# Kernel tuning notes

Measured on AMD Instinct MI355X. Metric: run time of the kernel, lower is better.

The kernel has to match this reference:

```python
import jax, jax.numpy as jnp
import numpy as np

EPS = 1e-8  # torch F.cosine_similarity eps


def _gather(features, idx):
    # batched_index_select_tensor: per-batch gather along seq dim
    return jnp.take_along_axis(features, idx[:, :, None], axis=1)


def setup_inputs() -> dict:
    key = jax.random.key(0)
    ks = jax.random.split(key, 7)
    B, S, H, Q, D, C = 8, 512, 768, 64, 256, 2
    return {
        "features": jax.random.normal(ks[0], (B, S, H), dtype=jnp.float32),
        "text_a_indices": jax.random.randint(ks[1], (B, Q), 0, S),
        "text_b_indices": jax.random.randint(ks[2], (B, D), 0, S),
        "W1": jax.random.normal(ks[3], (2 * H, H), dtype=jnp.float32) * 0.02,
        "b1": jax.random.normal(ks[4], (H,), dtype=jnp.float32) * 0.02,
        "W2": jax.random.normal(ks[5], (H, C), dtype=jnp.float32) * 0.02,
        "b2": jax.random.normal(ks[6], (C,), dtype=jnp.float32) * 0.02,
    }


def reference(features, text_a_indices, text_b_indices, W1, b1, W2, b2):
    dt = features.dtype
    a_mask = (text_a_indices > 0).astype(dt)          # [B,Q]
    b_mask = (text_b_indices > 0).astype(dt)          # [B,D]
    a_len = jnp.sum(a_mask, axis=-1)                  # [B]
    b_len = jnp.sum(b_mask, axis=-1)                  # [B]

    q_vec = _gather(features, text_a_indices)         # [B,Q,H]
    d_vec = _gather(features, text_b_indices)         # [B,D,H]

    # cosine similarity with torch eps semantics: x.y / (max(|x|,eps)*max(|y|,eps))
    qn = q_vec / jnp.maximum(jnp.linalg.norm(q_vec, axis=-1, keepdims=True), EPS)
    dn = d_vec / jnp.maximum(jnp.linalg.norm(d_vec, axis=-1, keepdims=True), EPS)
    sim = jnp.einsum("bqh,bdh->bqd", qn, dn)          # [B,Q,D]

    # masked weighted average over doc tokens, per query token (fused; no 4D repeat)
    sim_m = sim * b_mask[:, None, :]
    per_q_doc = jnp.einsum("bqd,bdh->bqh", sim_m, d_vec) / b_len[:, None, None]

    # masked average over query tokens
    am = a_mask[:, :, None]
    query_based_doc = jnp.sum(per_q_doc * am, axis=1) / a_len[:, None]   # [B,H]
    query_avg = jnp.sum(q_vec * am, axis=1) / a_len[:, None]             # [B,H]

    feat = jnp.concatenate([query_avg, query_based_doc], axis=-1)        # [B,2H]
    hidden = jax.nn.relu(feat @ W1 + b1)
    logits = hidden @ W2 + b2
    return logits
```

## Files before the change

### kernel.cpp

```cpp
#include <hip/hip_runtime.h>
#include <hip/hip_bf16.h>

#define B_ 8
#define S_ 512
#define H_ 768
#define Q_ 64
#define D_ 256

#define WS_QBAR   0
#define WS_QA     (B_ * H_)
#define WS_W      (2 * B_ * H_)
#define WS_HIDDEN (2 * B_ * H_ + B_ * D_)
#define WS_CNT    (WS_HIDDEN + B_ * H_)
#define ZERO_N    (B_ * H_ + 256)

__global__ __launch_bounds__(256) void k_qbar(
        const float* __restrict__ feats,
        const int* __restrict__ aidx,
        float* __restrict__ ws) {
    float* qbar = ws + WS_QBAR;
    float* qa   = ws + WS_QA;
    int b = blockIdx.x / 12, hc = blockIdx.x % 12;
    int t = threadIdx.x, wv = t >> 6, lane = t & 63;
    __shared__ float s_alen;
    __shared__ float red0[4][64], red1[4][64];
    if (wv == 0) {
        unsigned long long ma = __ballot(aidx[b * Q_ + lane] > 0);
        if (lane == 0) s_alen = (float)__popcll(ma);
    }
    int hh = hc * 64 + lane;
    float pb = 0.f, pa = 0.f;
#pragma unroll 2
    for (int q = wv * 16; q < wv * 16 + 16; ++q) {
        int idx = aidx[b * Q_ + q];
        const float* row = feats + ((size_t)b * S_ + idx) * H_;
        const float4* row4 = (const float4*)row;
        float ss = 0.f;
#pragma unroll
        for (int k = 0; k < 3; ++k) {
            float4 v = row4[lane + k * 64];
            ss += v.x * v.x + v.y * v.y + v.z * v.z + v.w * v.w;
        }
        for (int off = 32; off; off >>= 1) ss += __shfl_xor(ss, off, 64);
        float inv = 1.f / fmaxf(sqrtf(ss), 1e-8f);
        float f = row[hh];
        if (idx > 0) { pb += f * inv; pa += f; }
    }
    red0[wv][lane] = pb;
    red1[wv][lane] = pa;
    __syncthreads();
    if (t < 64) {
        int h2 = hc * 64 + t;
        float qb = red0[0][t] + red0[1][t] + red0[2][t] + red0[3][t];
        float qv = red1[0][t] + red1[1][t] + red1[2][t] + red1[3][t];
        qbar[b * H_ + h2] = qb;
        qa[b * H_ + h2] = qv / s_alen;
    }
}

__global__ __launch_bounds__(256) void k_docw(
        const float* __restrict__ feats,
        const int* __restrict__ aidx,
        const int* __restrict__ bidx,
        float* __restrict__ ws) {
    const float* qbar = ws + WS_QBAR;
    float* w = ws + WS_W;
    float* zero_region = ws + WS_HIDDEN;
    int t = threadIdx.x, wv = t >> 6, lane = t & 63;
    if (blockIdx.x < 25) {
        zero_region[blockIdx.x * 256 + t] = 0.f;
    }
    int gw = blockIdx.x * 4 + wv;
    int b = gw >> 8, d = gw & 255;
    __shared__ int cnt[4];
    __shared__ float s_alen;
    unsigned long long mb = __ballot(bidx[b * D_ + wv * 64 + lane] > 0);
    if (lane == 0) cnt[wv] = __popcll(mb);
    if (wv == 0) {
        unsigned long long ma = __ballot(aidx[b * Q_ + lane] > 0);
        if (lane == 0) s_alen = (float)__popcll(ma);
    }
    __syncthreads();
    float blen = (float)(cnt[0] + cnt[1] + cnt[2] + cnt[3]);
    int idx = bidx[b * D_ + d];
    const float4* row4 = (const float4*)(feats + ((size_t)b * S_ + idx) * H_);
    const float4* q4 = (const float4*)(qbar + b * H_);
    float dqf = 0.f, dff = 0.f;
#pragma unroll
    for (int k = 0; k < 3; ++k) {
        float4 v = row4[lane + k * 64];
        float4 qv = q4[lane + k * 64];
        dqf += v.x * qv.x + v.y * qv.y + v.z * qv.z + v.w * qv.w;
        dff += v.x * v.x + v.y * v.y + v.z * v.z + v.w * v.w;
    }
    for (int off = 32; off; off >>= 1) {
        dqf += __shfl_xor(dqf, off, 64);
        dff += __shfl_xor(dff, off, 64);
    }
    if (lane == 0) {
        float inv = 1.f / fmaxf(sqrtf(dff), 1e-8f);
        float scale = 1.f / (s_alen * blen);
        w[b * D_ + d] = (idx > 0) ? dqf * inv * scale : 0.f;
    }
}

__global__ __launch_bounds__(256) void k_docsum_mlp(
        const float* __restrict__ feats,
        const int* __restrict__ bidx,
        const float* __restrict__ W1,
        const float* __restrict__ b1,
        const float* __restrict__ W2,
        const float* __restrict__ b2,
        float* __restrict__ ws,
        float* __restrict__ out) {
    const float* qa = ws + WS_QA;
    const float* w  = ws + WS_W;
    float* hidden   = ws + WS_HIDDEN;
    int* counter    = (int*)(ws + WS_CNT);
    int b = blockIdx.x / 12, hc = blockIdx.x % 12;
    int t = threadIdx.x, wv = t >> 6, lane = t & 63;
    __shared__ float s_w[D_];
    __shared__ int   s_i[D_];
    __shared__ float s_k[128];
    __shared__ float red[4][64];
    __shared__ int   s_flag;
    s_w[t] = w[b * D_ + t];
    s_i[t] = bidx[b * D_ + t];
    if (t < 64) s_k[t] = qa[b * H_ + hc * 64 + t];
    __syncthreads();
    int hh = hc * 64 + lane;
    float acc = 0.f;
#pragma unroll 8
    for (int d = wv * 64; d < wv * 64 + 64; ++d)
        acc += s_w[d] * feats[((size_t)b * S_ + s_i[d]) * H_ + hh];
    red[wv][lane] = acc;
    __syncthreads();
    if (t < 64) s_k[64 + t] = red[0][t] + red[1][t] + red[2][t] + red[3][t];
    __syncthreads();
    const float* Wtop = W1 + (size_t)(hc * 64) * H_;
    const float* Wbot = W1 + (size_t)(H_ + hc * 64) * H_;
    float h0 = 0.f, h1 = 0.f, h2 = 0.f;
#pragma unroll 4
    for (int i = 0; i < 64; ++i) {
        float ka = s_k[i], kb = s_k[64 + i];
        const float* r1 = Wtop + (size_t)i * H_;
        const float* r2 = Wbot + (size_t)i * H_;
        h0 += ka * r1[t]       + kb * r2[t];
        h1 += ka * r1[t + 256] + kb * r2[t + 256];
        h2 += ka * r1[t + 512] + kb * r2[t + 512];
    }
    atomicAdd(&hidden[b * H_ + t],       h0);
    atomicAdd(&hidden[b * H_ + t + 256], h1);
    atomicAdd(&hidden[b * H_ + t + 512], h2);
    __threadfence();
    __syncthreads();
    if (t == 0) {
        int old = atomicAdd(counter, 1);
        s_flag = (old == 95);
    }
    __syncthreads();
    if (s_flag) {
        __threadfence();
        for (int bb = wv * 2; bb < wv * 2 + 2; ++bb) {
            float a0 = 0.f, a1 = 0.f;
#pragma unroll
            for (int k = 0; k < 12; ++k) {
                int h = lane + k * 64;
                float hv = __hip_atomic_load(&hidden[bb * H_ + h],
                                             __ATOMIC_RELAXED,
                                             __HIP_MEMORY_SCOPE_AGENT);
                float v = fmaxf(hv + b1[h], 0.f);
                a0 += v * W2[h * 2 + 0];
                a1 += v * W2[h * 2 + 1];
            }
            for (int off = 32; off; off >>= 1) {
                a0 += __shfl_xor(a0, off, 64);
                a1 += __shfl_xor(a1, off, 64);
            }
            if (lane == 0) {
                out[bb * 2 + 0] = a0 + b2[0];
                out[bb * 2 + 1] = a1 + b2[1];
            }
        }
    }
}

extern "C" void kernel_launch(void* const* d_in, const int* in_sizes, int n_in,
                              void* d_out, int out_size, void* d_ws, size_t ws_size,
                              hipStream_t stream) {
    const float* feats = (const float*)d_in[0];
    const int*   aidx  = (const int*)d_in[1];
    const int*   bidx  = (const int*)d_in[2];
    const float* W1    = (const float*)d_in[3];
    const float* b1    = (const float*)d_in[4];
    const float* W2    = (const float*)d_in[5];
    const float* b2    = (const float*)d_in[6];
    float* out = (float*)d_out;
    float* ws = (float*)d_ws;

    k_qbar<<<96, 256, 0, stream>>>(feats, aidx, ws);
    k_docw<<<512, 256, 0, stream>>>(feats, aidx, bidx, ws);
    k_docsum_mlp<<<96, 256, 0, stream>>>(feats, bidx, W1, b1, W2, b2, ws, out);
}
```

Measured before the change: 113.3 us.

## Fuse query, doc-weight and MLP stages into one kernel with redundant per-block work

Merges the three kernels into a single 512-thread kernel per (batch, hidden-chunk) block. Each block recomputes the full query-norm sum and all 256 doc weights itself rather than reading them from workspace written by earlier launches. The atomic hidden accumulation and last-block counter are replaced by per-chunk partial sums that a small tail kernel reduces. This removes launch overhead, the atomics and the workspace zeroing, at the cost of each batch's gathers being repeated 12 times across blocks.

```diff
diff --git a/kernel.cpp b/kernel.cpp
--- a/kernel.cpp
+++ b/kernel.cpp
@@ -6,182 +6,172 @@
 #define H_ 768
 #define Q_ 64
 #define D_ 256
+#define EPSF 1e-8f
 
-#define WS_QBAR   0
-#define WS_QA     (B_ * H_)
-#define WS_W      (2 * B_ * H_)
-#define WS_HIDDEN (2 * B_ * H_ + B_ * D_)
-#define WS_CNT    (WS_HIDDEN + B_ * H_)
-#define ZERO_N    (B_ * H_ + 256)
-
-__global__ __launch_bounds__(256) void k_qbar(
+__global__ __launch_bounds__(512) void k_main(
         const float* __restrict__ feats,
         const int* __restrict__ aidx,
-        float* __restrict__ ws) {
-    float* qbar = ws + WS_QBAR;
-    float* qa   = ws + WS_QA;
-    int b = blockIdx.x / 12, hc = blockIdx.x % 12;
-    int t = threadIdx.x, wv = t >> 6, lane = t & 63;
+        const int* __restrict__ bidx,
+        const float* __restrict__ W1,
+        float* __restrict__ partial) {
+    const int b = blockIdx.x / 12, hc = blockIdx.x % 12;
+    const int t = threadIdx.x, wv = t >> 6, lane = t & 63;
+
+    __shared__ __align__(16) float s_qbar[H_];
+    __shared__ float s_k[128];
+    __shared__ float s_w[D_];
+    __shared__ float s_inv[Q_], s_m[Q_];
+    __shared__ int   s_ai[Q_], s_bi[D_];
+    __shared__ float red[8][64];
+    __shared__ int   s_cnt[4];
     __shared__ float s_alen;
-    __shared__ float red0[4][64], red1[4][64];
+
+    if (t < Q_) s_ai[t] = aidx[b * Q_ + t];
+    if (t >= 256) s_bi[t - 256] = bidx[b * D_ + (t - 256)];
+    __syncthreads();
+
     if (wv == 0) {
-        unsigned long long ma = __ballot(aidx[b * Q_ + lane] > 0);
+        unsigned long long ma = __ballot(s_ai[lane] > 0);
         if (lane == 0) s_alen = (float)__popcll(ma);
+    } else if (wv >= 4) {
+        unsigned long long mb = __ballot(s_bi[(wv - 4) * 64 + lane] > 0);
+        if (lane == 0) s_cnt[wv - 4] = __popcll(mb);
     }
-    int hh = hc * 64 + lane;
-    float pb = 0.f, pa = 0.f;
+
+    for (int j = 0; j < 8; ++j) {
+        int q = wv * 8 + j;
+        int idx = s_ai[q];
+        const float4* row4 = (const float4*)(feats + (size_t)(b * S_ + idx) * H_);
+        float4 v0 = row4[lane], v1 = row4[lane + 64], v2 = row4[lane + 128];
+        float ss = v0.x*v0.x + v0.y*v0.y + v0.z*v0.z + v0.w*v0.w
+                 + v1.x*v1.x + v1.y*v1.y + v1.z*v1.z + v1.w*v1.w
+                 + v2.x*v2.x + v2.y*v2.y + v2.z*v2.z + v2.w*v2.w;
+        for (int off = 32; off; off >>= 1) ss += __shfl_xor(ss, off, 64);
+        if (lane == 0) {
+            float inv = 1.f / fmaxf(sqrtf(ss), EPSF);
+            s_inv[q] = (idx > 0) ? inv : 0.f;
+            s_m[q]   = (idx > 0) ? 1.f : 0.f;
+        }
+    }
+    __syncthreads();
+
+    {
+        float accb0 = 0.f, acca0 = 0.f, accb1 = 0.f, acca1 = 0.f;
+#pragma unroll 8
+        for (int q = 0; q < Q_; ++q) {
+            const float* row = feats + (size_t)(b * S_ + s_ai[q]) * H_;
+            float iv = s_inv[q], mv = s_m[q];
+            float f0 = row[t];
+            accb0 += f0 * iv; acca0 += f0 * mv;
+            if (t < 256) {
+                float f1 = row[512 + t];
+                accb1 += f1 * iv; acca1 += f1 * mv;
+            }
+        }
+        s_qbar[t] = accb0;
+        if (t < 256) s_qbar[512 + t] = accb1;
+        int c0 = t - hc * 64;
+        if (c0 >= 0 && c0 < 64) s_k[c0] = acca0 / s_alen;
+        if (t < 256) {
+            int c1 = 512 + t - hc * 64;
+            if (c1 >= 0 && c1 < 64) s_k[c1] = acca1 / s_alen;
+        }
+    }
+    __syncthreads();
+
+    {
+        const float4* q4 = (const float4*)s_qbar;
+        float4 qb0 = q4[lane], qb1 = q4[lane + 64], qb2 = q4[lane + 128];
+        float blen = (float)(s_cnt[0] + s_cnt[1] + s_cnt[2] + s_cnt[3]);
+        float scale = 1.f / (s_alen * blen);
 #pragma unroll 2
-    for (int q = wv * 16; q < wv * 16 + 16; ++q) {
-        int idx = aidx[b * Q_ + q];
-        const float* row = feats + ((size_t)b * S_ + idx) * H_;
-        const float4* row4 = (const float4*)row;
-        float ss = 0.f;
-#pragma unroll
-        for (int k = 0; k < 3; ++k) {
-            float4 v = row4[lane + k * 64];
-            ss += v.x * v.x + v.y * v.y + v.z * v.z + v.w * v.w;
+        for (int j = 0; j < 32; ++j) {
+            int d = wv * 32 + j;
+            int idx = s_bi[d];
+            const float4* row4 = (const float4*)(feats + (size_t)(b * S_ + idx) * H_);
+            float4 v0 = row4[lane], v1 = row4[lane + 64], v2 = row4[lane + 128];
+            float dqf = v0.x*qb0.x + v0.y*qb0.y + v0.z*qb0.z + v0.w*qb0.w
+                      + v1.x*qb1.x + v1.y*qb1.y + v1.z*qb1.z + v1.w*qb1.w
+                      + v2.x*qb2.x + v2.y*qb2.y + v2.z*qb2.z + v2.w*qb2.w;
+            float dff = v0.x*v0.x + v0.y*v0.y + v0.z*v0.z + v0.w*v0.w
+                      + v1.x*v1.x + v1.y*v1.y + v1.z*v1.z + v1.w*v1.w
+                      + v2.x*v2.x + v2.y*v2.y + v2.z*v2.z + v2.w*v2.w;
+            for (int off = 32; off; off >>= 1) {
+                dqf += __shfl_xor(dqf, off, 64);
+                dff += __shfl_xor(dff, off, 64);
+            }
+            if (lane == 0) {
+                float invd = 1.f / fmaxf(sqrtf(dff), EPSF);
+                s_w[d] = (idx > 0) ? dqf * invd * scale : 0.f;
+            }
         }
-        for (int off = 32; off; off >>= 1) ss += __shfl_xor(ss, off, 64);
-        float inv = 1.f / fmaxf(sqrtf(ss), 1e-8f);
-        float f = row[hh];
-        if (idx > 0) { pb += f * inv; pa += f; }
     }
-    red0[wv][lane] = pb;
-    red1[wv][lane] = pa;
+    __syncthreads();
+
+    {
+        float acc = 0.f;
+#pragma unroll 4
+        for (int j = 0; j < 32; ++j) {
+            int d = wv * 32 + j;
+            acc += s_w[d] * feats[(size_t)(b * S_ + s_bi[d]) * H_ + hc * 64 + lane];
+        }
+        red[wv][lane] = acc;
+    }
     __syncthreads();
     if (t < 64) {
-        int h2 = hc * 64 + t;
-        float qb = red0[0][t] + red0[1][t] + red0[2][t] + red0[3][t];
-        float qv = red1[0][t] + red1[1][t] + red1[2][t] + red1[3][t];
-        qbar[b * H_ + h2] = qb;
-        qa[b * H_ + h2] = qv / s_alen;
+        float q = 0.f;
+#pragma unroll
+        for (int w8 = 0; w8 < 8; ++w8) q += red[w8][t];
+        s_k[64 + t] = q;
+    }
+    __syncthreads();
+
+    {
+        const float* Wtop = W1 + (size_t)(hc * 64) * H_;
+        const float* Wbot = W1 + (size_t)(H_ + hc * 64) * H_;
+        float acc0 = 0.f, acc1 = 0.f;
+#pragma unroll 4
+        for (int i = 0; i < 64; ++i) {
+            float ka = s_k[i], kb = s_k[64 + i];
+            const float* r1 = Wtop + (size_t)i * H_;
+            const float* r2 = Wbot + (size_t)i * H_;
+            acc0 += ka * r1[t] + kb * r2[t];
+            if (t < 256) acc1 += ka * r1[512 + t] + kb * r2[512 + t];
+        }
+        float* po = partial + (size_t)(hc * B_ + b) * H_;
+        po[t] = acc0;
+        if (t < 256) po[512 + t] = acc1;
     }
 }
 
-__global__ __launch_bounds__(256) void k_docw(
-        const float* __restrict__ feats,
-        const int* __restrict__ aidx,
-        const int* __restrict__ bidx,
-        float* __restrict__ ws) {
-    const float* qbar = ws + WS_QBAR;
-    float* w = ws + WS_W;
-    float* zero_region = ws + WS_HIDDEN;
-    int t = threadIdx.x, wv = t >> 6, lane = t & 63;
-    if (blockIdx.x < 25) {
-        zero_region[blockIdx.x * 256 + t] = 0.f;
-    }
-    int gw = blockIdx.x * 4 + wv;
-    int b = gw >> 8, d = gw & 255;
-    __shared__ int cnt[4];
-    __shared__ float s_alen;
-    unsigned long long mb = __ballot(bidx[b * D_ + wv * 64 + lane] > 0);
-    if (lane == 0) cnt[wv] = __popcll(mb);
-    if (wv == 0) {
-        unsigned long long ma = __ballot(aidx[b * Q_ + lane] > 0);
-        if (lane == 0) s_alen = (float)__popcll(ma);
-    }
-    __syncthreads();
-    float blen = (float)(cnt[0] + cnt[1] + cnt[2] + cnt[3]);
-    int idx = bidx[b * D_ + d];
-    const float4* row4 = (const float4*)(feats + ((size_t)b * S_ + idx) * H_);
-    const float4* q4 = (const float4*)(qbar + b * H_);
-    float dqf = 0.f, dff = 0.f;
-#pragma unroll
-    for (int k = 0; k < 3; ++k) {
-        float4 v = row4[lane + k * 64];
-        float4 qv = q4[lane + k * 64];
-        dqf += v.x * qv.x + v.y * qv.y + v.z * qv.z + v.w * qv.w;
-        dff += v.x * v.x + v.y * v.y + v.z * v.z + v.w * v.w;
-    }
-    for (int off = 32; off; off >>= 1) {
-        dqf += __shfl_xor(dqf, off, 64);
-        dff += __shfl_xor(dff, off, 64);
-    }
-    if (lane == 0) {
-        float inv = 1.f / fmaxf(sqrtf(dff), 1e-8f);
-        float scale = 1.f / (s_alen * blen);
-        w[b * D_ + d] = (idx > 0) ? dqf * inv * scale : 0.f;
-    }
-}
-
-__global__ __launch_bounds__(256) void k_docsum_mlp(
-        const float* __restrict__ feats,
-        const int* __restrict__ bidx,
-        const float* __restrict__ W1,
+__global__ __launch_bounds__(256) void k_tail(
+        const float* __restrict__ partial,
         const float* __restrict__ b1,
         const float* __restrict__ W2,
         const float* __restrict__ b2,
-        float* __restrict__ ws,
         float* __restrict__ out) {
-    const float* qa = ws + WS_QA;
-    const float* w  = ws + WS_W;
-    float* hidden   = ws + WS_HIDDEN;
-    int* counter    = (int*)(ws + WS_CNT);
-    int b = blockIdx.x / 12, hc = blockIdx.x % 12;
-    int t = threadIdx.x, wv = t >> 6, lane = t & 63;
-    __shared__ float s_w[D_];
-    __shared__ int   s_i[D_];
-    __shared__ float s_k[128];
-    __shared__ float red[4][64];
-    __shared__ int   s_flag;
-    s_w[t] = w[b * D_ + t];
-    s_i[t] = bidx[b * D_ + t];
-    if (t < 64) s_k[t] = qa[b * H_ + hc * 64 + t];
-    __syncthreads();
-    int hh = hc * 64 + lane;
-    float acc = 0.f;
-#pragma unroll 8
-    for (int d = wv * 64; d < wv * 64 + 64; ++d)
-        acc += s_w[d] * feats[((size_t)b * S_ + s_i[d]) * H_ + hh];
-    red[wv][lane] = acc;
-    __syncthreads();
-    if (t < 64) s_k[64 + t] = red[0][t] + red[1][t] + red[2][t] + red[3][t];
-    __syncthreads();
-    const float* Wtop = W1 + (size_t)(hc * 64) * H_;
-    const float* Wbot = W1 + (size_t)(H_ + hc * 64) * H_;
-    float h0 = 0.f, h1 = 0.f, h2 = 0.f;
-#pragma unroll 4
-    for (int i = 0; i < 64; ++i) {
-        float ka = s_k[i], kb = s_k[64 + i];
-        const float* r1 = Wtop + (size_t)i * H_;
-        const float* r2 = Wbot + (size_t)i * H_;
-        h0 += ka * r1[t]       + kb * r2[t];
-        h1 += ka * r1[t + 256] + kb * r2[t + 256];
-        h2 += ka * r1[t + 512] + kb * r2[t + 512];
+    int b = blockIdx.x, t = threadIdx.x, lane = t & 63, wv = t >> 6;
+    float a0 = b1[t], a1 = b1[t + 256], a2 = b1[t + 512];
+#pragma unroll
+    for (int hc = 0; hc < 12; ++hc) {
+        const float* p = partial + (size_t)(hc * B_ + b) * H_;
+        a0 += p[t]; a1 += p[t + 256]; a2 += p[t + 512];
     }
-    atomicAdd(&hidden[b * H_ + t],       h0);
-    atomicAdd(&hidden[b * H_ + t + 256], h1);
-    atomicAdd(&hidden[b * H_ + t + 512], h2);
-    __threadfence();
+    a0 = fmaxf(a0, 0.f); a1 = fmaxf(a1, 0.f); a2 = fmaxf(a2, 0.f);
+    const float2* W22 = (const float2*)W2;
+    float2 w0 = W22[t], w1 = W22[t + 256], w2 = W22[t + 512];
+    float p0 = a0 * w0.x + a1 * w1.x + a2 * w2.x;
+    float p1 = a0 * w0.y + a1 * w1.y + a2 * w2.y;
+    for (int off = 32; off; off >>= 1) {
+        p0 += __shfl_xor(p0, off, 64);
+        p1 += __shfl_xor(p1, off, 64);
+    }
+    __shared__ float r0[4], r1[4];
+    if (lane == 0) { r0[wv] = p0; r1[wv] = p1; }
     __syncthreads();
     if (t == 0) {
-        int old = atomicAdd(counter, 1);
-        s_flag = (old == 95);
-    }
-    __syncthreads();
-    if (s_flag) {
-        __threadfence();
-        for (int bb = wv * 2; bb < wv * 2 + 2; ++bb) {
-            float a0 = 0.f, a1 = 0.f;
-#pragma unroll
-            for (int k = 0; k < 12; ++k) {
-                int h = lane + k * 64;
-                float hv = __hip_atomic_load(&hidden[bb * H_ + h],
-                                             __ATOMIC_RELAXED,
-                                             __HIP_MEMORY_SCOPE_AGENT);
-                float v = fmaxf(hv + b1[h], 0.f);
-                a0 += v * W2[h * 2 + 0];
-                a1 += v * W2[h * 2 + 1];
-            }
-            for (int off = 32; off; off >>= 1) {
-                a0 += __shfl_xor(a0, off, 64);
-                a1 += __shfl_xor(a1, off, 64);
-            }
-            if (lane == 0) {
-                out[bb * 2 + 0] = a0 + b2[0];
-                out[bb * 2 + 1] = a1 + b2[1];
-            }
-        }
+        out[b * 2 + 0] = r0[0] + r0[1] + r0[2] + r0[3] + b2[0];
+        out[b * 2 + 1] = r1[0] + r1[1] + r1[2] + r1[3] + b2[1];
     }
 }
 
@@ -196,9 +186,9 @@
     const float* W2    = (const float*)d_in[5];
     const float* b2    = (const float*)d_in[6];
     float* out = (float*)d_out;
-    float* ws = (float*)d_ws;
 
-    k_qbar<<<96, 256, 0, stream>>>(feats, aidx, ws);
-    k_docw<<<512, 256, 0, stream>>>(feats, aidx, bidx, ws);
-    k_docsum_mlp<<<96, 256, 0, stream>>>(feats, bidx, W1, b1, W2, b2, ws, out);
+    float* partial = (float*)d_ws;
+
+    k_main<<<96, 512, 0, stream>>>(feats, aidx, bidx, W1, partial);
+    k_tail<<<8, 256, 0, stream>>>(partial, b1, W2, b2, out);
 }
```

Result: slower. 135.1 us (+19.3%).

## Split query-mean kernel across more blocks and precompute doc norms in parallel

Applied to the files above, without the earlier changes.

Replaces the first kernel with a wider pre-pass of 256 blocks of 512 threads. Query-token reductions are split into two halves written as partial sums, and doc-token inverse norms are computed in the same launch. The doc-weight kernel then reads the precomputed inverse norms and sums the two query partials instead of recomputing norms. The aim is more parallelism in the first stage and less work in the second. In exchange there are extra workspace partials and small extra reads in the downstream kernels.

```diff
diff --git a/kernel.cpp b/kernel.cpp
--- a/kernel.cpp
+++ b/kernel.cpp
@@ -6,55 +6,86 @@
 #define H_ 768
 #define Q_ 64
 #define D_ 256
-
-#define WS_QBAR   0
-#define WS_QA     (B_ * H_)
-#define WS_W      (2 * B_ * H_)
-#define WS_HIDDEN (2 * B_ * H_ + B_ * D_)
+#define EPSF 1e-8f
+
+#define WS_INVD   0
+#define WS_QBARP  (B_ * D_)
+#define WS_QAP    (WS_QBARP + 2 * B_ * H_)
+#define WS_W      (WS_QAP + 2 * B_ * H_)
+#define WS_HIDDEN (WS_W + B_ * D_)
 #define WS_CNT    (WS_HIDDEN + B_ * H_)
-#define ZERO_N    (B_ * H_ + 256)
-
-__global__ __launch_bounds__(256) void k_qbar(
+
+__global__ __launch_bounds__(512) void k_pre(
         const float* __restrict__ feats,
         const int* __restrict__ aidx,
+        const int* __restrict__ bidx,
         float* __restrict__ ws) {
-    float* qbar = ws + WS_QBAR;
-    float* qa   = ws + WS_QA;
-    int b = blockIdx.x / 12, hc = blockIdx.x % 12;
-    int t = threadIdx.x, wv = t >> 6, lane = t & 63;
-    __shared__ float s_alen;
-    __shared__ float red0[4][64], red1[4][64];
-    if (wv == 0) {
-        unsigned long long ma = __ballot(aidx[b * Q_ + lane] > 0);
-        if (lane == 0) s_alen = (float)__popcll(ma);
-    }
-    int hh = hc * 64 + lane;
-    float pb = 0.f, pa = 0.f;
-#pragma unroll 2
-    for (int q = wv * 16; q < wv * 16 + 16; ++q) {
-        int idx = aidx[b * Q_ + q];
-        const float* row = feats + ((size_t)b * S_ + idx) * H_;
-        const float4* row4 = (const float4*)row;
-        float ss = 0.f;
-#pragma unroll
-        for (int k = 0; k < 3; ++k) {
-            float4 v = row4[lane + k * 64];
-            ss += v.x * v.x + v.y * v.y + v.z * v.z + v.w * v.w;
-        }
-        for (int off = 32; off; off >>= 1) ss += __shfl_xor(ss, off, 64);
-        float inv = 1.f / fmaxf(sqrtf(ss), 1e-8f);
-        float f = row[hh];
-        if (idx > 0) { pb += f * inv; pa += f; }
-    }
-    red0[wv][lane] = pb;
-    red1[wv][lane] = pa;
-    __syncthreads();
-    if (t < 64) {
-        int h2 = hc * 64 + t;
-        float qb = red0[0][t] + red0[1][t] + red0[2][t] + red0[3][t];
-        float qv = red1[0][t] + red1[1][t] + red1[2][t] + red1[3][t];
-        qbar[b * H_ + h2] = qb;
-        qa[b * H_ + h2] = qv / s_alen;
+    float* invd      = ws + WS_INVD;
+    float* qbar_part = ws + WS_QBARP;
+    float* qa_part   = ws + WS_QAP;
+    const int t = threadIdx.x, wv = t >> 6, lane = t & 63;
+
+    if (blockIdx.x < 192) {
+        const int b = blockIdx.x / 24, rem = blockIdx.x % 24;
+        const int hc = rem >> 1, qg = rem & 1;
+        __shared__ int   s_ai[32];
+        __shared__ float s_inv[32], s_m[32];
+        __shared__ float red0[8][64], red1[8][64];
+        if (t < 32) s_ai[t] = aidx[b * Q_ + qg * 32 + t];
+        __syncthreads();
+#pragma unroll
+        for (int j = 0; j < 4; ++j) {
+            int q = wv * 4 + j;
+            int idx = s_ai[q];
+            const float4* row4 = (const float4*)(feats + (size_t)(b * S_ + idx) * H_);
+            float4 v0 = row4[lane], v1 = row4[lane + 64], v2 = row4[lane + 128];
+            float ss = v0.x*v0.x + v0.y*v0.y + v0.z*v0.z + v0.w*v0.w
+                     + v1.x*v1.x + v1.y*v1.y + v1.z*v1.z + v1.w*v1.w
+                     + v2.x*v2.x + v2.y*v2.y + v2.z*v2.z + v2.w*v2.w;
+            for (int off = 32; off; off >>= 1) ss += __shfl_xor(ss, off, 64);
+            if (lane == 0) {
+                float inv = 1.f / fmaxf(sqrtf(ss), EPSF);
+                s_inv[q] = (idx > 0) ? inv : 0.f;
+                s_m[q]   = (idx > 0) ? 1.f : 0.f;
+            }
+        }
+        __syncthreads();
+        int h = hc * 64 + lane;
+        float pb = 0.f, pa = 0.f;
+#pragma unroll
+        for (int j = 0; j < 4; ++j) {
+            int q = wv * 4 + j;
+            const float* row = feats + (size_t)(b * S_ + s_ai[q]) * H_;
+            float f = row[h];
+            pb += f * s_inv[q];
+            pa += f * s_m[q];
+        }
+        red0[wv][lane] = pb;
+        red1[wv][lane] = pa;
+        __syncthreads();
+        if (t < 64) {
+            float sb = 0.f, sa = 0.f;
+#pragma unroll
+            for (int k = 0; k < 8; ++k) { sb += red0[k][t]; sa += red1[k][t]; }
+            qbar_part[(size_t)(qg * B_ + b) * H_ + hc * 64 + t] = sb;
+            qa_part[(size_t)(qg * B_ + b) * H_ + hc * 64 + t]   = sa;
+        }
+    } else {
+        int gw = (blockIdx.x - 192) * 8 + wv;
+#pragma unroll
+        for (int j = 0; j < 4; ++j) {
+            int g = gw * 4 + j;
+            int b = g >> 8, d = g & 255;
+            int idx = bidx[b * D_ + d];
+            const float4* row4 = (const float4*)(feats + (size_t)(b * S_ + idx) * H_);
+            float4 v0 = row4[lane], v1 = row4[lane + 64], v2 = row4[lane + 128];
+            float ss = v0.x*v0.x + v0.y*v0.y + v0.z*v0.z + v0.w*v0.w
+                     + v1.x*v1.x + v1.y*v1.y + v1.z*v1.z + v1.w*v1.w
+                     + v2.x*v2.x + v2.y*v2.y + v2.z*v2.z + v2.w*v2.w;
+            for (int off = 32; off; off >>= 1) ss += __shfl_xor(ss, off, 64);
+            if (lane == 0)
+                invd[b * D_ + d] = (idx > 0) ? 1.f / fmaxf(sqrtf(ss), EPSF) : 0.f;
+        }
     }
 }
 
@@ -63,13 +94,12 @@
         const int* __restrict__ aidx,
         const int* __restrict__ bidx,
         float* __restrict__ ws) {
-    const float* qbar = ws + WS_QBAR;
-    float* w = ws + WS_W;
-    float* zero_region = ws + WS_HIDDEN;
-    int t = threadIdx.x, wv = t >> 6, lane = t & 63;
-    if (blockIdx.x < 25) {
-        zero_region[blockIdx.x * 256 + t] = 0.f;
-    }
+    const float* invd      = ws + WS_INVD;
+    const float* qbar_part = ws + WS_QBARP;
+    float* w               = ws + WS_W;
+    float* zero_region     = ws + WS_HIDDEN;
+    const int t = threadIdx.x, wv = t >> 6, lane = t & 63;
+    if (blockIdx.x < 25) zero_region[blockIdx.x * 256 + t] = 0.f;
     int gw = blockIdx.x * 4 + wv;
     int b = gw >> 8, d = gw & 255;
     __shared__ int cnt[4];
@@ -83,29 +113,26 @@
     __syncthreads();
     float blen = (float)(cnt[0] + cnt[1] + cnt[2] + cnt[3]);
     int idx = bidx[b * D_ + d];
-    const float4* row4 = (const float4*)(feats + ((size_t)b * S_ + idx) * H_);
-    const float4* q4 = (const float4*)(qbar + b * H_);
-    float dqf = 0.f, dff = 0.f;
+    const float4* row4 = (const float4*)(feats + (size_t)(b * S_ + idx) * H_);
+    const float4* q0 = (const float4*)(qbar_part + (size_t)b * H_);
+    const float4* q1 = (const float4*)(qbar_part + (size_t)(B_ + b) * H_);
+    float dqf = 0.f;
 #pragma unroll
     for (int k = 0; k < 3; ++k) {
-        float4 v = row4[lane + k * 64];
-        float4 qv = q4[lane + k * 64];
-        dqf += v.x * qv.x + v.y * qv.y + v.z * qv.z + v.w * qv.w;
-        dff += v.x * v.x + v.y * v.y + v.z * v.z + v.w * v.w;
-    }
-    for (int off = 32; off; off >>= 1) {
-        dqf += __shfl_xor(dqf, off, 64);
-        dff += __shfl_xor(dff, off, 64);
-    }
-    if (lane == 0) {
-        float inv = 1.f / fmaxf(sqrtf(dff), 1e-8f);
-        float scale = 1.f / (s_alen * blen);
-        w[b * D_ + d] = (idx > 0) ? dqf * inv * scale : 0.f;
-    }
+        float4 v  = row4[lane + k * 64];
+        float4 qa = q0[lane + k * 64];
+        float4 qb = q1[lane + k * 64];
+        dqf += v.x * (qa.x + qb.x) + v.y * (qa.y + qb.y)
+             + v.z * (qa.z + qb.z) + v.w * (qa.w + qb.w);
+    }
+    for (int off = 32; off; off >>= 1) dqf += __shfl_xor(dqf, off, 64);
+    if (lane == 0)
+        w[b * D_ + d] = dqf * invd[b * D_ + d] / (s_alen * blen);
 }
 
 __global__ __launch_bounds__(256) void k_docsum_mlp(
         const float* __restrict__ feats,
+        const int* __restrict__ aidx,
         const int* __restrict__ bidx,
         const float* __restrict__ W1,
         const float* __restrict__ b1,
@@ -113,26 +140,34 @@
         const float* __restrict__ b2,
         float* __restrict__ ws,
         float* __restrict__ out) {
-    const float* qa = ws + WS_QA;
-    const float* w  = ws + WS_W;
-    float* hidden   = ws + WS_HIDDEN;
-    int* counter    = (int*)(ws + WS_CNT);
-    int b = blockIdx.x / 12, hc = blockIdx.x % 12;
-    int t = threadIdx.x, wv = t >> 6, lane = t & 63;
+    const float* qa_part = ws + WS_QAP;
+    const float* w       = ws + WS_W;
+    float* hidden        = ws + WS_HIDDEN;
+    int* counter         = (int*)(ws + WS_CNT);
+    const int b = blockIdx.x / 12, hc = blockIdx.x % 12;
+    const int t = threadIdx.x, wv = t >> 6, lane = t & 63;
     __shared__ float s_w[D_];
     __shared__ int   s_i[D_];
     __shared__ float s_k[128];
     __shared__ float red[4][64];
+    __shared__ float s_alen;
     __shared__ int   s_flag;
     s_w[t] = w[b * D_ + t];
     s_i[t] = bidx[b * D_ + t];
-    if (t < 64) s_k[t] = qa[b * H_ + hc * 64 + t];
-    __syncthreads();
+    if (wv == 0) {
+        unsigned long long ma = __ballot(aidx[b * Q_ + lane] > 0);
+        if (lane == 0) s_alen = (float)__popcll(ma);
+    }
+    __syncthreads();
+    if (t < 64) {
+        s_k[t] = (qa_part[(size_t)b * H_ + hc * 64 + t]
+                + qa_part[(size_t)(B_ + b) * H_ + hc * 64 + t]) / s_alen;
+    }
     int hh = hc * 64 + lane;
     float acc = 0.f;
 #pragma unroll 8
     for (int d = wv * 64; d < wv * 64 + 64; ++d)
-        acc += s_w[d] * feats[((size_t)b * S_ + s_i[d]) * H_ + hh];
+        acc += s_w[d] * feats[(size_t)(b * S_ + s_i[d]) * H_ + hh];
     red[wv][lane] = acc;
     __syncthreads();
     if (t < 64) s_k[64 + t] = red[0][t] + red[1][t] + red[2][t] + red[3][t];
@@ -198,7 +233,7 @@
     float* out = (float*)d_out;
     float* ws = (float*)d_ws;
 
-    k_qbar<<<96, 256, 0, stream>>>(feats, aidx, ws);
+    k_pre<<<256, 512, 0, stream>>>(feats, aidx, bidx, ws);
     k_docw<<<512, 256, 0, stream>>>(feats, aidx, bidx, ws);
-    k_docsum_mlp<<<96, 256, 0, stream>>>(feats, bidx, W1, b1, W2, b2, ws, out);
-}
+    k_docsum_mlp<<<96, 256, 0, stream>>>(feats, aidx, bidx, W1, b1, W2, b2, ws, out);
+}
```

After: 102.9 us. 1.1x faster.
